# Performance work log

Hardware: AMD Instinct MI355X
Metric: run time of the kernel (lower is better)

The kernel has to match this reference:

```python
import jax, jax.numpy as jnp
from jax import lax
import numpy as np

B, T, H, K = 32, 512, 2048, 128


def setup_inputs() -> dict:
    key = jax.random.key(0)
    k1, k2, k3, k4, k5, k6, k7 = jax.random.split(key, 7)
    hiddens = jax.random.normal(k1, (B, T, H), dtype=jnp.float32)
    mask = jnp.ones((B, T), dtype=jnp.int32)  # mask[:,0] must be on (torchcrf)
    labels = jax.random.randint(k2, (B, T), 0, K)
    W = jax.random.normal(k3, (H, K), dtype=jnp.float32) * 0.02
    b = jnp.zeros((K,), dtype=jnp.float32)
    # torchcrf inits transitions uniform(-0.1, 0.1)
    start_transitions = jax.random.uniform(k4, (K,), minval=-0.1, maxval=0.1)
    end_transitions = jax.random.uniform(k5, (K,), minval=-0.1, maxval=0.1)
    transitions = jax.random.uniform(k6, (K, K), minval=-0.1, maxval=0.1)
    return {"hiddens": hiddens, "mask": mask, "labels": labels, "W": W, "b": b,
            "start_transitions": start_transitions, "end_transitions": end_transitions,
            "transitions": transitions}


def _crf_log_likelihood(emissions, tags, mask, start_t, end_t, trans):
    # emissions: [B,T,K], tags/mask: [B,T]
    Bn, Tn, Kn = emissions.shape
    maskf = mask.astype(emissions.dtype)
    # ---- numerator: score of the gold path ----
    score = start_t[tags[:, 0]] + emissions[jnp.arange(Bn), 0, tags[:, 0]]
    prev, cur = tags[:, :-1], tags[:, 1:]
    emit_cur = jnp.take_along_axis(emissions[:, 1:], cur[..., None], axis=-1)[..., 0]
    score = score + jnp.sum((trans[prev, cur] + emit_cur) * maskf[:, 1:], axis=1)
    last_idx = mask.sum(axis=1).astype(jnp.int32) - 1
    last_tags = jnp.take_along_axis(tags, last_idx[:, None], axis=1)[:, 0]
    score = score + end_t[last_tags]
    # ---- denominator: log partition via stable logsumexp scan ----
    def step(alpha, inp):
        emit_t, m_t = inp  # [B,K], [B]
        nxt = jax.nn.logsumexp(alpha[:, :, None] + trans[None] + emit_t[:, None, :], axis=1)
        alpha = jnp.where(m_t[:, None] > 0, nxt, alpha)
        return alpha, None
    alpha0 = start_t[None, :] + emissions[:, 0]
    emits = jnp.swapaxes(emissions[:, 1:], 0, 1)  # [T-1,B,K]
    ms = jnp.swapaxes(mask[:, 1:], 0, 1)          # [T-1,B]
    alpha, _ = lax.scan(step, alpha0, (emits, ms))
    logZ = jax.nn.logsumexp(alpha + end_t[None, :], axis=1)
    return score - logZ


def _viterbi_decode(emissions, mask, start_t, end_t, trans):
    Bn, Tn, Kn = emissions.shape
    tag_ids = jnp.arange(Kn, dtype=jnp.int32)
    def step(score, inp):
        emit_t, m_t = inp
        cand = score[:, :, None] + trans[None]          # [B,K,K] prev->cur
        bp = jnp.argmax(cand, axis=1).astype(jnp.int32)  # [B,K]
        best = jnp.max(cand, axis=1) + emit_t
        on = m_t[:, None] > 0
        new_score = jnp.where(on, best, score)
        bp = jnp.where(on, bp, tag_ids[None, :])  # identity for padded steps
        return new_score, bp
    score0 = start_t[None, :] + emissions[:, 0]
    emits = jnp.swapaxes(emissions[:, 1:], 0, 1)
    ms = jnp.swapaxes(mask[:, 1:], 0, 1)
    score, history = lax.scan(step, score0, (emits, ms))  # history: [T-1,B,K]
    last_tag = jnp.argmax(score + end_t[None, :], axis=1).astype(jnp.int32)  # [B]
    def back(tag, bp_t):
        tag = jnp.take_along_axis(bp_t, tag[:, None], axis=1)[:, 0]
        return tag, tag
    _, tags_prev = lax.scan(back, last_tag, history, reverse=True)  # [T-1,B]
    tags = jnp.concatenate([tags_prev, last_tag[None, :]], axis=0)  # [T,B]
    return jnp.swapaxes(tags, 0, 1)  # [B,T]


def reference(hiddens, mask, labels, W, b, start_transitions, end_transitions, transitions):
    logits = jnp.einsum('bth,hk->btk', hiddens, W) + b  # emission projection
    decode = _viterbi_decode(logits, mask, start_transitions, end_transitions, transitions)
    llh = _crf_log_likelihood(logits, labels, mask, start_transitions, end_transitions, transitions)
    loss = -jnp.mean(llh)  # -1 * crf(..., reduction='mean')
    return (decode, loss)
```

## Files before the change

kernel.cpp:

```cpp
#include <hip/hip_runtime.h>
#include <hip/hip_bf16.h>
#include <math.h>

#define BB 32
#define TT 512
#define HH 2048
#define KK 128
#define CH 8
#define NC 32
#define NCV 64

#define WS_LOGITS 0
#define WS_SHIST  8388608u
#define WS_BP     16777216u

__device__ __forceinline__ float quad_add(float x) {
    int a = __builtin_amdgcn_update_dpp(0, __float_as_int(x), 0xB1, 0xF, 0xF, true);
    x += __int_as_float(a);
    int b = __builtin_amdgcn_update_dpp(0, __float_as_int(x), 0x4E, 0xF, 0xF, true);
    x += __int_as_float(b);
    return x;
}
__device__ __forceinline__ float quad_max(float x) {
    int a = __builtin_amdgcn_update_dpp(0, __float_as_int(x), 0xB1, 0xF, 0xF, true);
    x = fmaxf(x, __int_as_float(a));
    int b = __builtin_amdgcn_update_dpp(0, __float_as_int(x), 0x4E, 0xF, 0xF, true);
    x = fmaxf(x, __int_as_float(b));
    return x;
}

__device__ __forceinline__ void step_barrier() {
    __builtin_amdgcn_sched_barrier(0);
    asm volatile("s_waitcnt lgkmcnt(0)" ::: "memory");
    __builtin_amdgcn_sched_barrier(0);
    __builtin_amdgcn_s_barrier();
    __builtin_amdgcn_sched_barrier(0);
}

__global__ __launch_bounds__(512) void gemm_k(const float* __restrict__ hid,
                                              const float* __restrict__ Wm,
                                              const float* __restrict__ bias,
                                              float* __restrict__ logits,
                                              float* __restrict__ loss_slot) {
    __shared__ union {
        struct { float As[4][16][72]; float Bs[4][16][132]; } s;
        float4 red[16][128];
    } sm;
    const int tid = threadIdx.x, bid = blockIdx.x;
    if (bid == 0 && tid == 0) loss_slot[0] = 0.0f;
    const int g = tid >> 7, lt = tid & 127;
    const int rowBase = bid * 64;
    const int rowg = lt >> 4, colg = lt & 15;
    const int arow = lt >> 1, ahq = lt & 1;

    float acc[8][8];
#pragma unroll
    for (int i = 0; i < 8; i++)
#pragma unroll
        for (int j = 0; j < 8; j++) acc[i][j] = 0.0f;

    const float* hA = hid + (size_t)(rowBase + arow) * HH + g * 512 + ahq * 8;

    float4 a0, a1, bv[4];
    {
        const int h0 = g * 512;
        a0 = *(const float4*)(hA);
        a1 = *(const float4*)(hA + 4);
#pragma unroll
        for (int r = 0; r < 4; ++r) {
            int idx = r * 128 + lt;
            bv[r] = *(const float4*)(Wm + (size_t)(h0 + (idx >> 5)) * KK + (idx & 31) * 4);
        }
    }

    for (int it = 0; it < 32; ++it) {
        __syncthreads();
        const int hb = ahq * 8;
        sm.s.As[g][hb + 0][arow] = a0.x;
        sm.s.As[g][hb + 1][arow] = a0.y;
        sm.s.As[g][hb + 2][arow] = a0.z;
        sm.s.As[g][hb + 3][arow] = a0.w;
        sm.s.As[g][hb + 4][arow] = a1.x;
        sm.s.As[g][hb + 5][arow] = a1.y;
        sm.s.As[g][hb + 6][arow] = a1.z;
        sm.s.As[g][hb + 7][arow] = a1.w;
#pragma unroll
        for (int r = 0; r < 4; ++r) {
            int idx = r * 128 + lt;
            *(float4*)&sm.s.Bs[g][idx >> 5][(idx & 31) * 4] = bv[r];
        }
        __syncthreads();
        if (it + 1 < 32) {
            const int h0 = g * 512 + (it + 1) * 16;
            a0 = *(const float4*)(hA + (it + 1) * 16);
            a1 = *(const float4*)(hA + (it + 1) * 16 + 4);
#pragma unroll
            for (int r = 0; r < 4; ++r) {
                int idx = r * 128 + lt;
                bv[r] = *(const float4*)(Wm + (size_t)(h0 + (idx >> 5)) * KK + (idx & 31) * 4);
            }
        }
#pragma unroll
        for (int h = 0; h < 16; ++h) {
            float4 aL = *(const float4*)&sm.s.As[g][h][rowg * 8];
            float4 aH = *(const float4*)&sm.s.As[g][h][rowg * 8 + 4];
            float4 b0 = *(const float4*)&sm.s.Bs[g][h][colg * 4];
            float4 b1 = *(const float4*)&sm.s.Bs[g][h][64 + colg * 4];
            float ar[8] = {aL.x, aL.y, aL.z, aL.w, aH.x, aH.y, aH.z, aH.w};
            float br[8] = {b0.x, b0.y, b0.z, b0.w, b1.x, b1.y, b1.z, b1.w};
#pragma unroll
            for (int i = 0; i < 8; i++)
#pragma unroll
                for (int j = 0; j < 8; j++) acc[i][j] = fmaf(ar[i], br[j], acc[i][j]);
        }
    }
    __syncthreads();
    for (int gp = 1; gp <= 3; ++gp) {
        if (g == gp) {
#pragma unroll
            for (int i = 0; i < 8; ++i) {
                sm.red[i * 2][lt] = make_float4(acc[i][0], acc[i][1], acc[i][2], acc[i][3]);
                sm.red[i * 2 + 1][lt] = make_float4(acc[i][4], acc[i][5], acc[i][6], acc[i][7]);
            }
        }
        __syncthreads();
        if (g == 0) {
#pragma unroll
            for (int i = 0; i < 8; ++i) {
                float4 r0 = sm.red[i * 2][lt];
                float4 r1 = sm.red[i * 2 + 1][lt];
                acc[i][0] += r0.x; acc[i][1] += r0.y; acc[i][2] += r0.z; acc[i][3] += r0.w;
                acc[i][4] += r1.x; acc[i][5] += r1.y; acc[i][6] += r1.z; acc[i][7] += r1.w;
            }
        }
        __syncthreads();
    }
    if (g == 0) {
        float4 bb0 = *(const float4*)(bias + colg * 4);
        float4 bb1 = *(const float4*)(bias + 64 + colg * 4);
#pragma unroll
        for (int i = 0; i < 8; ++i) {
            int row = rowBase + rowg * 8 + i;
            *(float4*)(logits + (size_t)row * KK + colg * 4) =
                make_float4(acc[i][0] + bb0.x, acc[i][1] + bb0.y, acc[i][2] + bb0.z, acc[i][3] + bb0.w);
            *(float4*)(logits + (size_t)row * KK + 64 + colg * 4) =
                make_float4(acc[i][4] + bb1.x, acc[i][5] + bb1.y, acc[i][6] + bb1.z, acc[i][7] + bb1.w);
        }
    }
}

struct SMemB {
    float ubuf[2][144];
    float red[4];
};

__global__ __launch_bounds__(256, 1) void scan_k(const float* __restrict__ logits,
                                                 const int* __restrict__ mask,
                                                 const int* __restrict__ labels,
                                                 const float* __restrict__ startT,
                                                 const float* __restrict__ endT,
                                                 const float* __restrict__ trans,
                                                 float* __restrict__ shist,
                                                 float* __restrict__ out) {
    __shared__ SMemB sm;
    const int tid = threadIdx.x;
    const int bid = blockIdx.x;
    const float L2E = 1.4426950408889634f;
    const int s = tid & 3;
    const int jb = tid >> 2;
    const int j0 = jb * 2;
    const int padw = j0 + 4 * (j0 >> 5);
    const int lane = tid & 63;

    if (bid < BB) {
        const int b = bid;
        const float* lrow = logits + (size_t)b * TT * KK;
        unsigned long long mb[8];
#pragma unroll
        for (int c = 0; c < 8; ++c) mb[c] = __ballot(mask[b * TT + c * 64 + lane] != 0);
        float V0[32], V1[32];
#pragma unroll
        for (int k = 0; k < 32; k++) {
            V0[k] = exp2f(trans[(s * 32 + k) * KK + j0] * L2E);
            V1[k] = exp2f(trans[(s * 32 + k) * KK + j0 + 1] * L2E);
        }
        float a0_ = (startT[j0] + lrow[j0]) * L2E;
        float a1_ = (startT[j0 + 1] + lrow[j0 + 1]) * L2E;
        float OFF = (startT[0] + lrow[0]) * L2E;
        float S0_ = exp2f(a0_ - OFF);
        float S1_ = exp2f(a1_ - OFF);
        if (s == 0) {
            sm.ubuf[0][padw] = S0_;
            sm.ubuf[0][padw + 1] = S1_;
        }
        float2 emc[CH], emn[CH];
#pragma unroll
        for (int d = 0; d < CH; ++d) emc[d] = *(const float2*)(lrow + (size_t)d * KK + j0);
        __syncthreads();
        int cur = 0;
        for (int c = 0; c < NC; ++c) {
#pragma unroll
            for (int r = 0; r < CH; ++r) {
                const int t = c * CH + r;
                if (r == 0 && c + 1 < NC) {
#pragma unroll
                    for (int d = 0; d < CH; ++d)
                        emn[d] = *(const float2*)(lrow + (size_t)((c + 1) * CH + d) * KK + j0);
                }
                if (t > 0 && ((mb[t >> 6] >> (t & 63)) & 1ull)) {
                    const float* ub = &sm.ubuf[cur][s * 36];
                    float u00 = sm.ubuf[cur][0];
                    float uu[32];
#pragma unroll
                    for (int cc = 0; cc < 8; ++cc) {
                        float4 v = *(const float4*)(ub + cc * 4);
                        uu[cc * 4] = v.x; uu[cc * 4 + 1] = v.y; uu[cc * 4 + 2] = v.z; uu[cc * 4 + 3] = v.w;
                    }
                    float2 em = emc[r];
                    float p0e = 0.f, p0o = 0.f, p1e = 0.f, p1o = 0.f;
#pragma unroll
                    for (int k = 0; k < 32; k += 2) {
                        p0e = fmaf(uu[k], V0[k], p0e);
                        p1e = fmaf(uu[k], V1[k], p1e);
                        p0o = fmaf(uu[k + 1], V0[k + 1], p0o);
                        p1o = fmaf(uu[k + 1], V1[k + 1], p1o);
                    }
                    float w0 = quad_add(p0e + p0o);
                    float w1 = quad_add(p1e + p1o);
                    float rinv = __builtin_amdgcn_rcpf(u00);
                    OFF += log2f(u00);
                    S0_ = w0 * (exp2f(em.x * L2E) * rinv);
                    S1_ = w1 * (exp2f(em.y * L2E) * rinv);
                    if (s == 0) {
                        sm.ubuf[cur ^ 1][padw] = S0_;
                        sm.ubuf[cur ^ 1][padw + 1] = S1_;
                    }
                    cur ^= 1;
                }
                step_barrier();
            }
#pragma unroll
            for (int d = 0; d < CH; ++d) emc[d] = emn[d];
        }
        if (s == 0) {
            out[b * TT + j0] = S0_;
            out[b * TT + j0 + 1] = S1_;
        }
        if (tid == 0) out[b * TT + 384] = OFF;

        float part = 0.0f;
        for (int tt = tid; tt < TT; tt += 256) {
            if (tt == 0) {
                int l0 = labels[b * TT];
                part += startT[l0] + lrow[l0];
            } else if (mask[b * TT + tt]) {
                int lc = labels[b * TT + tt];
                int lp = labels[b * TT + tt - 1];
                part += trans[lp * KK + lc] + lrow[(size_t)tt * KK + lc];
            }
        }
#pragma unroll
        for (int d = 1; d < 64; d <<= 1) part += __shfl_xor(part, d, 64);
        int wid = tid >> 6;
        if (lane == 0) sm.red[wid] = part;
        __syncthreads();
        if (tid == 0) {
            int total = 0;
#pragma unroll
            for (int c = 0; c < 8; ++c) total += __popcll(mb[c]);
            float score = sm.red[0] + sm.red[1] + sm.red[2] + sm.red[3];
            score += endT[labels[b * TT + total - 1]];
            out[b * TT + 386] = score;
        }
    } else if (bid < 2 * BB) {
        const int b = bid - BB;
        const float* lrow = logits + (size_t)b * TT * KK;
        unsigned long long mb[4];
#pragma unroll
        for (int c = 0; c < 4; ++c) mb[c] = __ballot(mask[b * TT + 256 + c * 64 + lane] != 0);
        float V0[32], V1[32];
#pragma unroll
        for (int k = 0; k < 32; k++) {
            V0[k] = exp2f(trans[j0 * KK + s * 32 + k] * L2E);
            V1[k] = exp2f(trans[(j0 + 1) * KK + s * 32 + k] * L2E);
        }
        float OFF = endT[0] * L2E;
        float S0_ = exp2f(endT[j0] * L2E - OFF);
        float S1_ = exp2f(endT[j0 + 1] * L2E - OFF);
        {
            float2 e511 = *(const float2*)(lrow + (size_t)511 * KK + j0);
            if (s == 0) {
                sm.ubuf[0][padw] = exp2f(e511.x * L2E) * S0_;
                sm.ubuf[0][padw + 1] = exp2f(e511.y * L2E) * S1_;
            }
        }
        float2 emc[CH], emn[CH];
#pragma unroll
        for (int d = 0; d < CH; ++d) emc[d] = *(const float2*)(lrow + (size_t)(510 - d) * KK + j0);
        __syncthreads();
        int cur = 0;
        for (int c = 0; c < NC; ++c) {
#pragma unroll
            for (int r = 0; r < CH; ++r) {
                const int t = 511 - (c * CH + r);
                if (r == 0 && c + 1 < NC) {
#pragma unroll
                    for (int d = 0; d < CH; ++d)
                        emn[d] = *(const float2*)(lrow + (size_t)(510 - (c + 1) * CH - d) * KK + j0);
                }
                if ((mb[(t - 256) >> 6] >> ((t - 256) & 63)) & 1ull) {
                    const float* ub = &sm.ubuf[cur][s * 36];
                    float u00 = sm.ubuf[cur][0];
                    float uu[32];
#pragma unroll
                    for (int cc = 0; cc < 8; ++cc) {
                        float4 v = *(const float4*)(ub + cc * 4);
                        uu[cc * 4] = v.x; uu[cc * 4 + 1] = v.y; uu[cc * 4 + 2] = v.z; uu[cc * 4 + 3] = v.w;
                    }
                    float p0e = 0.f, p0o = 0.f, p1e = 0.f, p1o = 0.f;
#pragma unroll
                    for (int k = 0; k < 32; k += 2) {
                        p0e = fmaf(uu[k], V0[k], p0e);
                        p1e = fmaf(uu[k], V1[k], p1e);
                        p0o = fmaf(uu[k + 1], V0[k + 1], p0o);
                        p1o = fmaf(uu[k + 1], V1[k + 1], p1o);
                    }
                    float w0 = quad_add(p0e + p0o);
                    float w1 = quad_add(p1e + p1o);
                    float rinv = __builtin_amdgcn_rcpf(u00);
                    OFF += log2f(u00);
                    S0_ = w0 * rinv;
                    S1_ = w1 * rinv;
                }
                float2 em = emc[r];
                if (s == 0) {
                    sm.ubuf[cur ^ 1][padw] = exp2f(em.x * L2E) * S0_;
                    sm.ubuf[cur ^ 1][padw + 1] = exp2f(em.y * L2E) * S1_;
                }
                cur ^= 1;
                step_barrier();
            }
#pragma unroll
            for (int d = 0; d < CH; ++d) emc[d] = emn[d];
        }
        if (s == 0) {
            out[b * TT + 128 + j0] = S0_;
            out[b * TT + 128 + j0 + 1] = S1_;
        }
        if (tid == 0) out[b * TT + 385] = OFF;
    } else {
        const int b = bid - 2 * BB;
        const float* lrow = logits + (size_t)b * TT * KK;
        float* hist = shist + (size_t)b * TT * KK;
        unsigned long long mb[8];
#pragma unroll
        for (int c = 0; c < 8; ++c) mb[c] = __ballot(mask[b * TT + c * 64 + lane] != 0);
        float T0[32], T1[32];
#pragma unroll
        for (int k = 0; k < 32; k++) {
            T0[k] = trans[(s * 32 + k) * KK + j0];
            T1[k] = trans[(s * 32 + k) * KK + j0 + 1];
        }
        float s0_ = startT[j0] + lrow[j0];
        float s1_ = startT[j0 + 1] + lrow[j0 + 1];
        if (s == 0) {
            sm.ubuf[0][padw] = s0_;
            sm.ubuf[0][padw + 1] = s1_;
        } else if (s == 1) {
            *(float2*)(hist + j0) = make_float2(s0_, s1_);
        }
        float2 emc[CH], emn[CH], hb[CH];
#pragma unroll
        for (int d = 0; d < CH; ++d) emc[d] = *(const float2*)(lrow + (size_t)d * KK + j0);
        __syncthreads();
        int cur = 0;
        for (int c = 0; c < NCV; ++c) {
#pragma unroll
            for (int r = 0; r < CH; ++r) {
                const int t = c * CH + r;
                if (r == 0 && c + 1 < NCV) {
#pragma unroll
                    for (int d = 0; d < CH; ++d)
                        emn[d] = *(const float2*)(lrow + (size_t)((c + 1) * CH + d) * KK + j0);
                }
                if (t > 0 && ((mb[t >> 6] >> (t & 63)) & 1ull)) {
                    const float* ub = &sm.ubuf[cur][s * 36];
                    float uu[32];
#pragma unroll
                    for (int cc = 0; cc < 8; ++cc) {
                        float4 v = *(const float4*)(ub + cc * 4);
                        uu[cc * 4] = v.x; uu[cc * 4 + 1] = v.y; uu[cc * 4 + 2] = v.z; uu[cc * 4 + 3] = v.w;
                    }
                    float2 em = emc[r];
                    float m0a = -3.0e38f, m0b = -3.0e38f, m1a = -3.0e38f, m1b = -3.0e38f;
#pragma unroll
                    for (int k = 0; k < 32; k += 4) {
                        m0a = fmaxf(m0a, fmaxf(uu[k] + T0[k], uu[k + 1] + T0[k + 1]));
                        m0b = fmaxf(m0b, fmaxf(uu[k + 2] + T0[k + 2], uu[k + 3] + T0[k + 3]));
                        m1a = fmaxf(m1a, fmaxf(uu[k] + T1[k], uu[k + 1] + T1[k + 1]));
                        m1b = fmaxf(m1b, fmaxf(uu[k + 2] + T1[k + 2], uu[k + 3] + T1[k + 3]));
                    }
                    float m0 = quad_max(fmaxf(m0a, m0b));
                    float m1 = quad_max(fmaxf(m1a, m1b));
                    s0_ = m0 + em.x;
                    s1_ = m1 + em.y;
                    if (s == 0) {
                        sm.ubuf[cur ^ 1][padw] = s0_;
                        sm.ubuf[cur ^ 1][padw + 1] = s1_;
                    }
                    cur ^= 1;
                }
                hb[r] = make_float2(s0_, s1_);
                step_barrier();
            }
            if (s == 1) {
#pragma unroll
                for (int r = 0; r < CH; ++r)
                    *(float2*)(hist + (size_t)(c * CH + r) * KK + j0) = hb[r];
            }
#pragma unroll
            for (int d = 0; d < CH; ++d) emc[d] = emn[d];
        }
    }
}

__global__ __launch_bounds__(256) void bp_k(const float* __restrict__ shist,
                                            const float* __restrict__ trans,
                                            const int* __restrict__ mask,
                                            unsigned char* __restrict__ bp) {
    const int t = blockIdx.x + 1;
    const int tid = threadIdx.x;
    const int j = tid & 127, bg = tid >> 7;
    __shared__ float sc[BB][KK];
#pragma unroll
    for (int r = 0; r < 4; ++r) {
        int f = tid + r * 256;
        int bb2 = f >> 5, c4 = (f & 31) * 4;
        *(float4*)&sc[bb2][c4] = *(const float4*)&shist[(size_t)bb2 * TT * KK + (size_t)(t - 1) * KK + c4];
    }
    __syncthreads();
    float m[16];
    int idx[16];
#pragma unroll
    for (int c = 0; c < 16; c++) { m[c] = -3.0e38f; idx[c] = 0; }
    for (int i4 = 0; i4 < 32; ++i4) {
        const int ib = i4 * 4;
        float tr0 = trans[(ib + 0) * KK + j];
        float tr1 = trans[(ib + 1) * KK + j];
        float tr2 = trans[(ib + 2) * KK + j];
        float tr3 = trans[(ib + 3) * KK + j];
#pragma unroll
        for (int c = 0; c < 16; c++) {
            float4 s4 = *(const float4*)&sc[bg + 2 * c][ib];
            float c0 = s4.x + tr0, c1 = s4.y + tr1, c2 = s4.z + tr2, c3 = s4.w + tr3;
            if (c0 > m[c]) { m[c] = c0; idx[c] = ib; }
            if (c1 > m[c]) { m[c] = c1; idx[c] = ib + 1; }
            if (c2 > m[c]) { m[c] = c2; idx[c] = ib + 2; }
            if (c3 > m[c]) { m[c] = c3; idx[c] = ib + 3; }
        }
    }
#pragma unroll
    for (int c = 0; c < 16; c++) {
        int bb2 = bg + 2 * c;
        int v = idx[c];
        if (mask[bb2 * TT + t] == 0) v = j;
        bp[(size_t)bb2 * TT * KK + (size_t)t * KK + j] = (unsigned char)v;
    }
}

__global__ __launch_bounds__(512) void bt_k(const float* __restrict__ shist,
                                            const float* __restrict__ endT,
                                            const unsigned char* __restrict__ bp,
                                            float* __restrict__ out) {
    const int b = blockIdx.x;
    const int tid = threadIdx.x;
    const int lane = tid & 63, w = tid >> 6;
    __shared__ float cb[128];
    __shared__ float pb[128];
    __shared__ int tagbuf[512];
    __shared__ int handoff;
    if (tid < 128) {
        cb[tid] = shist[(size_t)b * TT * KK + (size_t)(TT - 1) * KK + tid] + endT[tid];
        pb[tid] = out[b * TT + tid] * out[b * TT + 128 + tid];
    }
    float offA = out[b * TT + 384];
    float offB = out[b * TT + 385];
    float score = out[b * TT + 386];
    unsigned int reg[64];
    const unsigned char* bpb = bp + (size_t)b * TT * KK;
#pragma unroll
    for (int r = 0; r < 64; r++) {
        int t_row = w * 64 + 1 + r;
        unsigned int v = 0;
        if (t_row < TT) v = *(const unsigned short*)(bpb + (size_t)t_row * KK + lane * 2);
        reg[r] = v;
    }
    __syncthreads();
    if (tid == 0) {
        float mm = cb[0];
        int bi = 0;
        for (int i = 1; i < 128; i++)
            if (cb[i] > mm) { mm = cb[i]; bi = i; }
        tagbuf[TT - 1] = bi;
        handoff = bi;
        float sum = 0.0f;
        for (int i = 0; i < 128; i++) sum += pb[i];
        float logZ = (offA + offB + log2f(sum)) * 0.6931471805599453f;
        float llh = score - logZ;
        atomicAdd(out + BB * TT, -llh * (1.0f / 32.0f));
    }
    __syncthreads();
    for (int ph = 7; ph >= 0; --ph) {
        if (w == ph) {
            int tag = handoff;
#pragma unroll
            for (int r = 63; r >= 0; --r) {
                int t_row = ph * 64 + 1 + r;
                if (t_row < TT) {
                    unsigned int vv = (unsigned int)__shfl((int)reg[r], tag >> 1, 64);
                    tag = (int)((vv >> ((tag & 1) * 8)) & 0xffu);
                    if (lane == 0) tagbuf[t_row - 1] = tag;
                }
            }
            if (lane == 0) handoff = tag;
        }
        __syncthreads();
    }
    out[b * TT + tid] = (float)tagbuf[tid];
}

extern "C" void kernel_launch(void* const* d_in, const int* in_sizes, int n_in,
                              void* d_out, int out_size, void* d_ws, size_t ws_size,
                              hipStream_t stream) {
    const float* hid = (const float*)d_in[0];
    const int* mask = (const int*)d_in[1];
    const int* labels = (const int*)d_in[2];
    const float* Wm = (const float*)d_in[3];
    const float* bias = (const float*)d_in[4];
    const float* startT = (const float*)d_in[5];
    const float* endT = (const float*)d_in[6];
    const float* trans = (const float*)d_in[7];
    float* out = (float*)d_out;
    char* ws = (char*)d_ws;

    float* logits = (float*)(ws + WS_LOGITS);
    float* shist = (float*)(ws + WS_SHIST);
    unsigned char* bp = (unsigned char*)(ws + WS_BP);

    gemm_k<<<256, 512, 0, stream>>>(hid, Wm, bias, logits, out + BB * TT);
    scan_k<<<96, 256, 0, stream>>>(logits, mask, labels, startT, endT, trans, shist, out);
    bp_k<<<TT - 1, 256, 0, stream>>>(shist, trans, mask, bp);
    bt_k<<<BB, 512, 0, stream>>>(shist, endT, bp, out);
}
```

Before: 623.6 us.

## Restructure Viterbi scan to broadcast scores via readlane and reduce partial maxes in LDS

The Viterbi forward scan in scan_k changes its work split. Before, each quad of lanes owned two output tags and read previous scores from an LDS buffer, finishing with DPP quad max reductions. Now each wave covers a 32-tag slice of the previous state. Scores are broadcast with readlane, every lane builds partial maxes for two output tags, and the four waves' partials are merged through a small LDS array after a barrier. The aim is to cut LDS reads and cross-lane shuffles per step, at the cost of many scalar readlanes and an LDS exchange on every step. The history writes are also spread across all lanes instead of one quarter.

```diff
diff --git a/kernel.cpp b/kernel.cpp
--- a/kernel.cpp
+++ b/kernel.cpp
@@ -21,12 +21,9 @@
     x += __int_as_float(b);
     return x;
 }
-__device__ __forceinline__ float quad_max(float x) {
-    int a = __builtin_amdgcn_update_dpp(0, __float_as_int(x), 0xB1, 0xF, 0xF, true);
-    x = fmaxf(x, __int_as_float(a));
-    int b = __builtin_amdgcn_update_dpp(0, __float_as_int(x), 0x4E, 0xF, 0xF, true);
-    x = fmaxf(x, __int_as_float(b));
-    return x;
+
+__device__ __forceinline__ float lane_f(float v, int k) {
+    return __int_as_float(__builtin_amdgcn_readlane(__float_as_int(v), k));
 }
 
 __device__ __forceinline__ void step_barrier() {
@@ -152,6 +149,7 @@
 struct SMemB {
     float ubuf[2][144];
     float red[4];
+    float pw[2][4][128];
 };
 
 __global__ __launch_bounds__(256, 1) void scan_k(const float* __restrict__ logits,
@@ -355,24 +353,18 @@
         unsigned long long mb[8];
 #pragma unroll
         for (int c = 0; c < 8; ++c) mb[c] = __ballot(mask[b * TT + c * 64 + lane] != 0);
-        float T0[32], T1[32];
-#pragma unroll
-        for (int k = 0; k < 32; k++) {
-            T0[k] = trans[(s * 32 + k) * KK + j0];
-            T1[k] = trans[(s * 32 + k) * KK + j0 + 1];
-        }
-        float s0_ = startT[j0] + lrow[j0];
-        float s1_ = startT[j0 + 1] + lrow[j0 + 1];
-        if (s == 0) {
-            sm.ubuf[0][padw] = s0_;
-            sm.ubuf[0][padw + 1] = s1_;
-        } else if (s == 1) {
-            *(float2*)(hist + j0) = make_float2(s0_, s1_);
-        }
-        float2 emc[CH], emn[CH], hb[CH];
-#pragma unroll
-        for (int d = 0; d < CH; ++d) emc[d] = *(const float2*)(lrow + (size_t)d * KK + j0);
-        __syncthreads();
+        const int w = tid >> 6;
+        const int lo = lane & 31;
+        const int jf = 32 * w + lo;
+        const int jp = 2 * lane;
+        float2 T01[32];
+#pragma unroll
+        for (int k = 0; k < 32; k++)
+            T01[k] = *(const float2*)&trans[(size_t)(32 * w + k) * KK + jp];
+        float u = startT[jf] + lrow[jf];
+        float emc[CH], emn[CH], hb[CH];
+#pragma unroll
+        for (int d = 0; d < CH; ++d) emc[d] = lrow[(size_t)d * KK + jf];
         int cur = 0;
         for (int c = 0; c < NCV; ++c) {
 #pragma unroll
@@ -381,42 +373,36 @@
                 if (r == 0 && c + 1 < NCV) {
 #pragma unroll
                     for (int d = 0; d < CH; ++d)
-                        emn[d] = *(const float2*)(lrow + (size_t)((c + 1) * CH + d) * KK + j0);
+                        emn[d] = lrow[(size_t)((c + 1) * CH + d) * KK + jf];
                 }
                 if (t > 0 && ((mb[t >> 6] >> (t & 63)) & 1ull)) {
-                    const float* ub = &sm.ubuf[cur][s * 36];
-                    float uu[32];
-#pragma unroll
-                    for (int cc = 0; cc < 8; ++cc) {
-                        float4 v = *(const float4*)(ub + cc * 4);
-                        uu[cc * 4] = v.x; uu[cc * 4 + 1] = v.y; uu[cc * 4 + 2] = v.z; uu[cc * 4 + 3] = v.w;
+                    float p0a = -3.0e38f, p0b = -3.0e38f, p1a = -3.0e38f, p1b = -3.0e38f;
+#pragma unroll
+                    for (int k = 0; k < 32; k += 2) {
+                        float ua = lane_f(u, k);
+                        float ub_ = lane_f(u, k + 1);
+                        p0a = fmaxf(p0a, ua + T01[k].x);
+                        p1a = fmaxf(p1a, ua + T01[k].y);
+                        p0b = fmaxf(p0b, ub_ + T01[k + 1].x);
+                        p1b = fmaxf(p1b, ub_ + T01[k + 1].y);
                     }
-                    float2 em = emc[r];
-                    float m0a = -3.0e38f, m0b = -3.0e38f, m1a = -3.0e38f, m1b = -3.0e38f;
-#pragma unroll
-                    for (int k = 0; k < 32; k += 4) {
-                        m0a = fmaxf(m0a, fmaxf(uu[k] + T0[k], uu[k + 1] + T0[k + 1]));
-                        m0b = fmaxf(m0b, fmaxf(uu[k + 2] + T0[k + 2], uu[k + 3] + T0[k + 3]));
-                        m1a = fmaxf(m1a, fmaxf(uu[k] + T1[k], uu[k + 1] + T1[k + 1]));
-                        m1b = fmaxf(m1b, fmaxf(uu[k + 2] + T1[k + 2], uu[k + 3] + T1[k + 3]));
-                    }
-                    float m0 = quad_max(fmaxf(m0a, m0b));
-                    float m1 = quad_max(fmaxf(m1a, m1b));
-                    s0_ = m0 + em.x;
-                    s1_ = m1 + em.y;
-                    if (s == 0) {
-                        sm.ubuf[cur ^ 1][padw] = s0_;
-                        sm.ubuf[cur ^ 1][padw + 1] = s1_;
-                    }
+                    *(float2*)&sm.pw[cur][w][jp] =
+                        make_float2(fmaxf(p0a, p0b), fmaxf(p1a, p1b));
+                    step_barrier();
+                    float q0 = sm.pw[cur][0][jf];
+                    float q1 = sm.pw[cur][1][jf];
+                    float q2 = sm.pw[cur][2][jf];
+                    float q3 = sm.pw[cur][3][jf];
+                    u = fmaxf(fmaxf(q0, q1), fmaxf(q2, q3)) + emc[r];
                     cur ^= 1;
                 }
-                hb[r] = make_float2(s0_, s1_);
-                step_barrier();
-            }
-            if (s == 1) {
-#pragma unroll
-                for (int r = 0; r < CH; ++r)
-                    *(float2*)(hist + (size_t)(c * CH + r) * KK + j0) = hb[r];
+                hb[r] = u;
+            }
+            {
+                const int rbase = (lane >> 5) * 4;
+#pragma unroll
+                for (int r2 = 0; r2 < 4; ++r2)
+                    hist[(size_t)(c * CH + rbase + r2) * KK + jf] = hb[rbase + r2];
             }
 #pragma unroll
             for (int d = 0; d < CH; ++d) emc[d] = emn[d];
```

Measured after the change: 624.1 us. Within noise of the previous version (+0.1%).

## Double-buffer GEMM shared tiles and use packed v2f FMA accumulation

Applied to the files above, without the earlier changes.

The emission-projection GEMM now keeps two shared-memory tile buffers, so the next tile is written while the current one is consumed. This cuts the two barriers per iteration to one. The inner product uses packed two-wide FMAs (v_pk_fma_f32) on vector accumulators, halving the FMA instruction count. Shared memory use doubles, which can lower occupancy, and the packed FMAs need the A value broadcast into pairs.

```diff
diff --git a/kernel.cpp b/kernel.cpp
--- a/kernel.cpp
+++ b/kernel.cpp
@@ -14,6 +14,8 @@
 #define WS_SHIST  8388608u
 #define WS_BP     16777216u
 
+typedef float v2f __attribute__((ext_vector_type(2)));
+
 __device__ __forceinline__ float quad_add(float x) {
     int a = __builtin_amdgcn_update_dpp(0, __float_as_int(x), 0xB1, 0xF, 0xF, true);
     x += __int_as_float(a);
@@ -43,7 +45,7 @@
                                               float* __restrict__ logits,
                                               float* __restrict__ loss_slot) {
     __shared__ union {
-        struct { float As[4][16][72]; float Bs[4][16][132]; } s;
+        struct { float As[2][4][16][72]; float Bs[2][4][16][132]; } s;
         float4 red[16][128];
     } sm;
     const int tid = threadIdx.x, bid = blockIdx.x;
@@ -53,11 +55,11 @@
     const int rowg = lt >> 4, colg = lt & 15;
     const int arow = lt >> 1, ahq = lt & 1;
 
-    float acc[8][8];
+    v2f acc[8][4];
 #pragma unroll
     for (int i = 0; i < 8; i++)
 #pragma unroll
-        for (int j = 0; j < 8; j++) acc[i][j] = 0.0f;
+        for (int j = 0; j < 4; j++) acc[i][j] = (v2f)(0.0f);
 
     const float* hA = hid + (size_t)(rowBase + arow) * HH + g * 512 + ahq * 8;
 
@@ -72,24 +74,26 @@
             bv[r] = *(const float4*)(Wm + (size_t)(h0 + (idx >> 5)) * KK + (idx & 31) * 4);
         }
     }
-
-    for (int it = 0; it < 32; ++it) {
-        __syncthreads();
+    {
         const int hb = ahq * 8;
-        sm.s.As[g][hb + 0][arow] = a0.x;
-        sm.s.As[g][hb + 1][arow] = a0.y;
-        sm.s.As[g][hb + 2][arow] = a0.z;
-        sm.s.As[g][hb + 3][arow] = a0.w;
-        sm.s.As[g][hb + 4][arow] = a1.x;
-        sm.s.As[g][hb + 5][arow] = a1.y;
-        sm.s.As[g][hb + 6][arow] = a1.z;
-        sm.s.As[g][hb + 7][arow] = a1.w;
+        sm.s.As[0][g][hb + 0][arow] = a0.x;
+        sm.s.As[0][g][hb + 1][arow] = a0.y;
+        sm.s.As[0][g][hb + 2][arow] = a0.z;
+        sm.s.As[0][g][hb + 3][arow] = a0.w;
+        sm.s.As[0][g][hb + 4][arow] = a1.x;
+        sm.s.As[0][g][hb + 5][arow] = a1.y;
+        sm.s.As[0][g][hb + 6][arow] = a1.z;
+        sm.s.As[0][g][hb + 7][arow] = a1.w;
 #pragma unroll
         for (int r = 0; r < 4; ++r) {
             int idx = r * 128 + lt;
-            *(float4*)&sm.s.Bs[g][idx >> 5][(idx & 31) * 4] = bv[r];
-        }
-        __syncthreads();
+            *(float4*)&sm.s.Bs[0][g][idx >> 5][(idx & 31) * 4] = bv[r];
+        }
+    }
+    __syncthreads();
+
+    for (int it = 0; it < 32; ++it) {
+        const int p = it & 1;
         if (it + 1 < 32) {
             const int h0 = g * 512 + (it + 1) * 16;
             a0 = *(const float4*)(hA + (it + 1) * 16);
@@ -102,16 +106,41 @@
         }
 #pragma unroll
         for (int h = 0; h < 16; ++h) {
-            float4 aL = *(const float4*)&sm.s.As[g][h][rowg * 8];
-            float4 aH = *(const float4*)&sm.s.As[g][h][rowg * 8 + 4];
-            float4 b0 = *(const float4*)&sm.s.Bs[g][h][colg * 4];
-            float4 b1 = *(const float4*)&sm.s.Bs[g][h][64 + colg * 4];
+            float4 aL = *(const float4*)&sm.s.As[p][g][h][rowg * 8];
+            float4 aH = *(const float4*)&sm.s.As[p][g][h][rowg * 8 + 4];
+            float4 b0 = *(const float4*)&sm.s.Bs[p][g][h][colg * 4];
+            float4 b1 = *(const float4*)&sm.s.Bs[p][g][h][64 + colg * 4];
             float ar[8] = {aL.x, aL.y, aL.z, aL.w, aH.x, aH.y, aH.z, aH.w};
-            float br[8] = {b0.x, b0.y, b0.z, b0.w, b1.x, b1.y, b1.z, b1.w};
-#pragma unroll
-            for (int i = 0; i < 8; i++)
-#pragma unroll
-                for (int j = 0; j < 8; j++) acc[i][j] = fmaf(ar[i], br[j], acc[i][j]);
+            v2f br[4];
+            br[0].x = b0.x; br[0].y = b0.y;
+            br[1].x = b0.z; br[1].y = b0.w;
+            br[2].x = b1.x; br[2].y = b1.y;
+            br[3].x = b1.z; br[3].y = b1.w;
+#pragma unroll
+            for (int i = 0; i < 8; i++) {
+                v2f av;
+                av.x = ar[i]; av.y = ar[i];
+#pragma unroll
+                for (int j = 0; j < 4; j++)
+                    acc[i][j] = __builtin_elementwise_fma(av, br[j], acc[i][j]);
+            }
+        }
+        if (it + 1 < 32) {
+            const int hb = ahq * 8;
+            sm.s.As[p ^ 1][g][hb + 0][arow] = a0.x;
+            sm.s.As[p ^ 1][g][hb + 1][arow] = a0.y;
+            sm.s.As[p ^ 1][g][hb + 2][arow] = a0.z;
+            sm.s.As[p ^ 1][g][hb + 3][arow] = a0.w;
+            sm.s.As[p ^ 1][g][hb + 4][arow] = a1.x;
+            sm.s.As[p ^ 1][g][hb + 5][arow] = a1.y;
+            sm.s.As[p ^ 1][g][hb + 6][arow] = a1.z;
+            sm.s.As[p ^ 1][g][hb + 7][arow] = a1.w;
+#pragma unroll
+            for (int r = 0; r < 4; ++r) {
+                int idx = r * 128 + lt;
+                *(float4*)&sm.s.Bs[p ^ 1][g][idx >> 5][(idx & 31) * 4] = bv[r];
+            }
+            __syncthreads();
         }
     }
     __syncthreads();
@@ -119,8 +148,8 @@
         if (g == gp) {
 #pragma unroll
             for (int i = 0; i < 8; ++i) {
-                sm.red[i * 2][lt] = make_float4(acc[i][0], acc[i][1], acc[i][2], acc[i][3]);
-                sm.red[i * 2 + 1][lt] = make_float4(acc[i][4], acc[i][5], acc[i][6], acc[i][7]);
+                sm.red[i * 2][lt] = make_float4(acc[i][0].x, acc[i][0].y, acc[i][1].x, acc[i][1].y);
+                sm.red[i * 2 + 1][lt] = make_float4(acc[i][2].x, acc[i][2].y, acc[i][3].x, acc[i][3].y);
             }
         }
         __syncthreads();
@@ -129,8 +158,8 @@
             for (int i = 0; i < 8; ++i) {
                 float4 r0 = sm.red[i * 2][lt];
                 float4 r1 = sm.red[i * 2 + 1][lt];
-                acc[i][0] += r0.x; acc[i][1] += r0.y; acc[i][2] += r0.z; acc[i][3] += r0.w;
-                acc[i][4] += r1.x; acc[i][5] += r1.y; acc[i][6] += r1.z; acc[i][7] += r1.w;
+                acc[i][0].x += r0.x; acc[i][0].y += r0.y; acc[i][1].x += r0.z; acc[i][1].y += r0.w;
+                acc[i][2].x += r1.x; acc[i][2].y += r1.y; acc[i][3].x += r1.z; acc[i][3].y += r1.w;
             }
         }
         __syncthreads();
@@ -142,9 +171,9 @@
         for (int i = 0; i < 8; ++i) {
             int row = rowBase + rowg * 8 + i;
             *(float4*)(logits + (size_t)row * KK + colg * 4) =
-                make_float4(acc[i][0] + bb0.x, acc[i][1] + bb0.y, acc[i][2] + bb0.z, acc[i][3] + bb0.w);
+                make_float4(acc[i][0].x + bb0.x, acc[i][0].y + bb0.y, acc[i][1].x + bb0.z, acc[i][1].y + bb0.w);
             *(float4*)(logits + (size_t)row * KK + 64 + colg * 4) =
-                make_float4(acc[i][4] + bb1.x, acc[i][5] + bb1.y, acc[i][6] + bb1.z, acc[i][7] + bb1.w);
+                make_float4(acc[i][2].x + bb1.x, acc[i][2].y + bb1.y, acc[i][3].x + bb1.z, acc[i][3].y + bb1.w);
         }
     }
 }
```

After: 1.163 ms. +86.5%, slower.

## Double-buffer GEMM shared tiles and load W directly to LDS

Applied to the files above, without the earlier changes.

The emission-projection GEMM now keeps two shared-memory buffers for the A and B tiles. W tiles are streamed with global_load_lds straight into the next buffer, while the hidden-state tile is written after compute, so only one barrier per iteration remains. This is meant to overlap global loads with FMAs and save the register staging and LDS write for W. It doubles LDS use, which may lower occupancy, and drops the B-tile padding, which may add bank conflicts. It also relies on the barrier to order the asynchronous LDS loads, with no explicit vmcnt wait.

```diff
diff --git a/kernel.cpp b/kernel.cpp
--- a/kernel.cpp
+++ b/kernel.cpp
@@ -14,6 +14,9 @@
 #define WS_SHIST  8388608u
 #define WS_BP     16777216u
 
+#define AS1 __attribute__((address_space(1)))
+#define AS3 __attribute__((address_space(3)))
+
 __device__ __forceinline__ float quad_add(float x) {
     int a = __builtin_amdgcn_update_dpp(0, __float_as_int(x), 0xB1, 0xF, 0xF, true);
     x += __int_as_float(a);
@@ -43,7 +46,7 @@
                                               float* __restrict__ logits,
                                               float* __restrict__ loss_slot) {
     __shared__ union {
-        struct { float As[4][16][72]; float Bs[4][16][132]; } s;
+        struct { float As[2][4][16][72]; float Bs[2][4][16][128]; } s;
         float4 red[16][128];
     } sm;
     const int tid = threadIdx.x, bid = blockIdx.x;
@@ -61,51 +64,52 @@
 
     const float* hA = hid + (size_t)(rowBase + arow) * HH + g * 512 + ahq * 8;
 
-    float4 a0, a1, bv[4];
+    float4 a0, a1;
     {
-        const int h0 = g * 512;
         a0 = *(const float4*)(hA);
         a1 = *(const float4*)(hA + 4);
+        const int hb = ahq * 8;
+        sm.s.As[0][g][hb + 0][arow] = a0.x;
+        sm.s.As[0][g][hb + 1][arow] = a0.y;
+        sm.s.As[0][g][hb + 2][arow] = a0.z;
+        sm.s.As[0][g][hb + 3][arow] = a0.w;
+        sm.s.As[0][g][hb + 4][arow] = a1.x;
+        sm.s.As[0][g][hb + 5][arow] = a1.y;
+        sm.s.As[0][g][hb + 6][arow] = a1.z;
+        sm.s.As[0][g][hb + 7][arow] = a1.w;
+        const float* wsrc = Wm + (size_t)(g * 512) * KK;
+        float* bdst = &sm.s.Bs[0][g][0][0];
 #pragma unroll
         for (int r = 0; r < 4; ++r) {
             int idx = r * 128 + lt;
-            bv[r] = *(const float4*)(Wm + (size_t)(h0 + (idx >> 5)) * KK + (idx & 31) * 4);
-        }
-    }
+            __builtin_amdgcn_global_load_lds(
+                (const AS1 float*)(wsrc + idx * 4),
+                (AS3 float*)(bdst + idx * 4), 16, 0, 0);
+        }
+    }
+    __syncthreads();
 
     for (int it = 0; it < 32; ++it) {
-        __syncthreads();
-        const int hb = ahq * 8;
-        sm.s.As[g][hb + 0][arow] = a0.x;
-        sm.s.As[g][hb + 1][arow] = a0.y;
-        sm.s.As[g][hb + 2][arow] = a0.z;
-        sm.s.As[g][hb + 3][arow] = a0.w;
-        sm.s.As[g][hb + 4][arow] = a1.x;
-        sm.s.As[g][hb + 5][arow] = a1.y;
-        sm.s.As[g][hb + 6][arow] = a1.z;
-        sm.s.As[g][hb + 7][arow] = a1.w;
-#pragma unroll
-        for (int r = 0; r < 4; ++r) {
-            int idx = r * 128 + lt;
-            *(float4*)&sm.s.Bs[g][idx >> 5][(idx & 31) * 4] = bv[r];
-        }
-        __syncthreads();
+        const int p = it & 1;
         if (it + 1 < 32) {
-            const int h0 = g * 512 + (it + 1) * 16;
+            const float* wsrc = Wm + (size_t)(g * 512 + (it + 1) * 16) * KK;
+            float* bdst = &sm.s.Bs[p ^ 1][g][0][0];
+#pragma unroll
+            for (int r = 0; r < 4; ++r) {
+                int idx = r * 128 + lt;
+                __builtin_amdgcn_global_load_lds(
+                    (const AS1 float*)(wsrc + idx * 4),
+                    (AS3 float*)(bdst + idx * 4), 16, 0, 0);
+            }
             a0 = *(const float4*)(hA + (it + 1) * 16);
             a1 = *(const float4*)(hA + (it + 1) * 16 + 4);
-#pragma unroll
-            for (int r = 0; r < 4; ++r) {
-                int idx = r * 128 + lt;
-                bv[r] = *(const float4*)(Wm + (size_t)(h0 + (idx >> 5)) * KK + (idx & 31) * 4);
-            }
         }
 #pragma unroll
         for (int h = 0; h < 16; ++h) {
-            float4 aL = *(const float4*)&sm.s.As[g][h][rowg * 8];
-            float4 aH = *(const float4*)&sm.s.As[g][h][rowg * 8 + 4];
-            float4 b0 = *(const float4*)&sm.s.Bs[g][h][colg * 4];
-            float4 b1 = *(const float4*)&sm.s.Bs[g][h][64 + colg * 4];
+            float4 aL = *(const float4*)&sm.s.As[p][g][h][rowg * 8];
+            float4 aH = *(const float4*)&sm.s.As[p][g][h][rowg * 8 + 4];
+            float4 b0 = *(const float4*)&sm.s.Bs[p][g][h][colg * 4];
+            float4 b1 = *(const float4*)&sm.s.Bs[p][g][h][64 + colg * 4];
             float ar[8] = {aL.x, aL.y, aL.z, aL.w, aH.x, aH.y, aH.z, aH.w};
             float br[8] = {b0.x, b0.y, b0.z, b0.w, b1.x, b1.y, b1.z, b1.w};
 #pragma unroll
@@ -113,8 +117,19 @@
 #pragma unroll
                 for (int j = 0; j < 8; j++) acc[i][j] = fmaf(ar[i], br[j], acc[i][j]);
         }
-    }
-    __syncthreads();
+        if (it + 1 < 32) {
+            const int hb = ahq * 8;
+            sm.s.As[p ^ 1][g][hb + 0][arow] = a0.x;
+            sm.s.As[p ^ 1][g][hb + 1][arow] = a0.y;
+            sm.s.As[p ^ 1][g][hb + 2][arow] = a0.z;
+            sm.s.As[p ^ 1][g][hb + 3][arow] = a0.w;
+            sm.s.As[p ^ 1][g][hb + 4][arow] = a1.x;
+            sm.s.As[p ^ 1][g][hb + 5][arow] = a1.y;
+            sm.s.As[p ^ 1][g][hb + 6][arow] = a1.z;
+            sm.s.As[p ^ 1][g][hb + 7][arow] = a1.w;
+        }
+        __syncthreads();
+    }
     for (int gp = 1; gp <= 3; ++gp) {
         if (g == gp) {
 #pragma unroll
```

Result: slower. 1.204 ms (+93.1%).
